# Kernel tuning notes

Hardware: AMD Instinct MI355X
Metric: run time of the kernel (lower is better)

Reference implementation:

```python
import jax, jax.numpy as jnp
import numpy as np
from jax import lax

EPS = 1e-5
TAU = 2.0
THR = 1.0

@jax.custom_vjp
def spike_fn(x):
    # torch.heaviside(x, 1.0): 1 where x >= 0, else 0
    return (x >= 0).astype(x.dtype)

def _spike_fwd(x):
    return spike_fn(x), x

def _spike_bwd(x, g):
    alpha = 4.0
    s = jax.nn.sigmoid(alpha * x)
    return (g * (1.0 - s) * s * alpha,)

spike_fn.defvjp(_spike_fwd, _spike_bwd)

def lif(x):
    # sequential membrane recurrence over dim 0 (time)
    def step(v, xt):
        v = v + (xt - v) / TAU
        s = spike_fn(v - THR)
        v = (1.0 - lax.stop_gradient(s)) * v
        return v, s
    _, spikes = lax.scan(step, jnp.zeros_like(x[0]), x)
    return spikes

def bn(x, p):
    # eval-mode BatchNorm2d; p = [weight, bias, mean, var], each [C]
    w, b, m, v = p
    inv = w / jnp.sqrt(v + EPS)
    return (x - m[None, :, None, None]) * inv[None, :, None, None] + b[None, :, None, None]

def bn_and_pad(x, p):
    # BN then pad 1 pixel on all sides with the BN-of-zero value
    w, b, m, v = p
    y = bn(x, p)
    pad_val = b - m * w / jnp.sqrt(v + EPS)  # [C]
    y = jnp.pad(y, ((0, 0), (0, 0), (1, 1), (1, 1)))
    pv = pad_val[None, :, None]  # broadcasts over batch and spatial
    y = y.at[:, :, 0, :].set(pv)
    y = y.at[:, :, -1, :].set(pv)
    y = y.at[:, :, :, 0].set(pv)
    y = y.at[:, :, :, -1].set(pv)
    return y

def branch(x, w1, dw, pw, bn3):
    # RepConv: 1x1 -> BNAndPad(1) -> depthwise3x3(valid) -> 1x1 -> BN, then outer BN
    C = x.shape[1]
    y = jnp.einsum('oc,bchw->bohw', w1, x)
    y = bn_and_pad(y, bn3[0])
    y = lax.conv_general_dilated(y, dw[:, None, :, :], (1, 1), 'VALID',
                                 dimension_numbers=('NCHW', 'OIHW', 'NCHW'),
                                 feature_group_count=C)
    y = jnp.einsum('oc,bchw->bohw', pw, y)
    y = bn(y, bn3[1])
    y = bn(y, bn3[2])
    return y

def _to_heads(t, B, N, h, d):
    # [B,C,H,W] -> [B,h,N,d]
    return t.reshape(B, h * d, N).transpose(0, 2, 1).reshape(B, N, h, d).transpose(0, 2, 1, 3)

def forward(x, q_w1, q_dw, q_pw, q_bn, k_w1, k_dw, k_pw, k_bn,
            v_w1, v_dw, v_pw, v_bn, p_w1, p_dw, p_pw, p_bn,
            num_heads=8):
    B, C, H, W = x.shape
    N = H * W
    h = num_heads
    d = C // h
    scale = float(d) ** -0.5

    xs = lif(x)
    q = lif(branch(xs, q_w1, q_dw, q_pw, q_bn))
    k = lif(branch(xs, k_w1, k_dw, k_pw, k_bn))
    v = lif(branch(xs, v_w1, v_dw, v_pw, v_bn))

    q = _to_heads(q, B, N, h, d)
    k = _to_heads(k, B, N, h, d)
    v = _to_heads(v, B, N, h, d)

    kv = jnp.einsum('bhnd,bhne->bhde', k, v)          # [B,h,d,d]
    o = jnp.einsum('bhnd,bhde->bhne', q, kv) * scale  # [B,h,N,d]
    o = o.transpose(0, 1, 3, 2).reshape(B, C, N)       # [B,C,N]
    o = lif(o)
    o = o.reshape(B, C, H, W)
    o = branch(o, p_w1, p_dw, p_pw, p_bn)
    return o.reshape(B, C, H, W)

def setup_inputs() -> dict:
    key = jax.random.key(0)
    ks = jax.random.split(key, 20)
    B, C, H, W = 8, 256, 64, 64
    s1 = 1.0 / np.sqrt(C)

    def make_bn(k):
        k1, k2, k3, k4 = jax.random.split(k, 4)
        w = 1.0 + 0.1 * jax.random.normal(k1, (3, C), jnp.float32)
        b = 0.1 * jax.random.normal(k2, (3, C), jnp.float32)
        m = 0.1 * jax.random.normal(k3, (3, C), jnp.float32)
        var = jax.random.uniform(k4, (3, C), jnp.float32, 0.5, 1.5)
        return jnp.stack([w, b, m, var], axis=1)  # [3,4,C]

    inp = {'x': jax.random.normal(ks[0], (B, C, H, W), jnp.float32)}
    for i, p in enumerate(['q', 'k', 'v', 'p']):
        kk = jax.random.split(ks[1 + i], 4)
        inp[p + '_w1'] = jax.random.normal(kk[0], (C, C), jnp.float32) * s1
        inp[p + '_dw'] = jax.random.normal(kk[1], (C, 3, 3), jnp.float32) * 0.3
        inp[p + '_pw'] = jax.random.normal(kk[2], (C, C), jnp.float32) * s1
        inp[p + '_bn'] = make_bn(kk[3])
    return inp

def reference(x, q_w1, q_dw, q_pw, q_bn, k_w1, k_dw, k_pw, k_bn,
              v_w1, v_dw, v_pw, v_bn, p_w1, p_dw, p_pw, p_bn):
    return forward(x, q_w1, q_dw, q_pw, q_bn, k_w1, k_dw, k_pw, k_bn,
                   v_w1, v_dw, v_pw, v_bn, p_w1, p_dw, p_pw, p_bn)
```

## Files before the change

### kernel.cpp

```cpp
#include <hip/hip_runtime.h>
#include <hip/hip_bf16.h>
#include <math.h>

#define T_ 8
#define C_ 256
#define N_ 4096
#define CN_ (C_ * N_)
#define EPSB 1e-5f

typedef unsigned long long u64;
typedef unsigned int u32;
typedef short bf16x8 __attribute__((ext_vector_type(8)));
typedef float f32x4 __attribute__((ext_vector_type(4)));

static __device__ __forceinline__ unsigned short f2bf(float f) {
    __hip_bfloat16 h = __float2bfloat16(f);
    return *(unsigned short*)&h;
}
static __device__ __forceinline__ float bf2f(unsigned short u) {
    u32 x = (u32)u << 16;
    return *(float*)&x;
}


__global__ __launch_bounds__(256) void lif_x_frag(const float* __restrict__ X,
                                                  unsigned short* __restrict__ ST) {
    int nb = blockIdx.x * 32;
    int c0 = blockIdx.y * 8;
    int tid = threadIdx.x;
    int nj = tid & 31, ci = tid >> 5;
    size_t base = (size_t)(c0 + ci) * N_ + nb + nj;
    __shared__ unsigned short Ls[8][34];
    int k32 = c0 >> 5, quad = (c0 >> 3) & 3;
    float v = 0.f;
#pragma unroll
    for (int t = 0; t < T_; t++) {
        float xt = X[(size_t)t * CN_ + base];
        v = v + (xt - v) / 2.0f;
        int s = (v - 1.0f >= 0.f) ? 1 : 0;
        Ls[ci][nj] = s ? (unsigned short)0x3F80 : (unsigned short)0;
        if (s) v = 0.f;
        __syncthreads();
        if (tid < 32) {
            int np = nb + tid;
            bf16x8 bs;
#pragma unroll
            for (int j = 0; j < 8; j++) bs[j] = (short)Ls[j][tid];
            *(bf16x8*)&ST[(size_t)t * CN_ +
                ((size_t)((np >> 4) * 8 + k32)) * 512 + (quad * 16 + (np & 15)) * 8] = bs;
        }
        __syncthreads();
    }
}

struct LArgs {
    const float* F[3];
    unsigned char* sq;
    u64* kbp;
    u64* vbp;
};
__global__ __launch_bounds__(256) void lif3(LArgs a) {
    int br = blockIdx.y;
    int idx = blockIdx.x * 256 + threadIdx.x;
    const float* X = a.F[br];
    int lane = threadIdx.x & 63;
    u64* BP = (br == 1) ? a.kbp : a.vbp;
    float v = 0.f;
#pragma unroll
    for (int t = 0; t < T_; t++) {
        float xt = X[(size_t)t * CN_ + idx];
        v = v + (xt - v) / 2.0f;
        int s = (v - 1.0f >= 0.f) ? 1 : 0;
        if (br == 0) {
            a.sq[(size_t)t * CN_ + idx] = (unsigned char)s;
        } else {
            u64 mask = __ballot(s);
            if (lane == 0) BP[((size_t)t * CN_ + idx) >> 6] = mask;
        }
        if (s) v = 0.f;
    }
}

struct WPtrs { const float* w[8]; };
__global__ __launch_bounds__(256) void split_w(WPtrs p, unsigned short* __restrict__ out) {
    int mat = blockIdx.y;
    int idx = blockIdx.x * 256 + threadIdx.x;
    int m = idx >> 8, k = idx & 255;
    float w = p.w[mat][idx];
    unsigned short h1 = f2bf(w);
    float f1 = bf2f(h1);
    unsigned short h2 = f2bf(w - f1);
    unsigned short h3 = f2bf(w - f1 - bf2f(h2));
    int lane = ((k >> 3) & 3) * 16 + (m & 15);
    size_t pos = ((size_t)(((m >> 4) * 8 + (k >> 5)) * 64 + lane)) * 8 + (k & 7);
    size_t base = (size_t)mat * 3 * 65536;
    out[base + pos] = h1;
    out[base + 65536 + pos] = h2;
    out[base + 2 * 65536 + pos] = h3;
}

static __device__ __forceinline__ void dw_body(const float* __restrict__ Yt,
                                               const float* __restrict__ dw,
                                               const float* __restrict__ bnp,
                                               unsigned short* __restrict__ Bh,
                                               unsigned short* __restrict__ Bl,
                                               int y0, int cg, int tid) {
    int c0 = cg * 8;
    __shared__ float L[8][6][68];
    __shared__ float invs[8], bs_[8], ms_[8], pads_[8];

    if (tid < 8) {
        int c = c0 + tid;
        float w = bnp[c], b = bnp[256 + c], m = bnp[512 + c], var = bnp[768 + c];
        float sq = sqrtf(var + EPSB);
        invs[tid] = w / sq;
        bs_[tid] = b;
        ms_[tid] = m;
        pads_[tid] = b - (m * w) / sq;
    }
    __syncthreads();

    for (int i = tid; i < 8 * 6 * 66; i += 256) {
        int c = i / 396;
        int rem = i - c * 396;
        int row = rem / 66, col = rem - row * 66;
        int gy = y0 - 1 + row, gx = col - 1;
        float val;
        if (gy < 0 || gy > 63 || gx < 0 || gx > 63) val = pads_[c];
        else val = (Yt[(size_t)(c0 + c) * N_ + gy * 64 + gx] - ms_[c]) * invs[c] + bs_[c];
        L[c][row][col] = val;
    }
    __syncthreads();

    int x = tid & 63, ry = tid >> 6;
    int n = (y0 + ry) * 64 + x;

    bf16x8 hi, lo;
#pragma unroll
    for (int j = 0; j < 8; j++) {
        const float* dwc = dw + (c0 + j) * 9;
        float a = 0.f;
#pragma unroll
        for (int dy = 0; dy < 3; dy++)
#pragma unroll
            for (int dx = 0; dx < 3; dx++)
                a += dwc[dy * 3 + dx] * L[j][ry + dy][x + dx];
        unsigned short h = f2bf(a);
        hi[j] = (short)h;
        lo[j] = (short)f2bf(a - bf2f(h));
    }
    size_t pos = ((size_t)((n >> 4) * 8 + (cg >> 2))) * 512 +
                 (size_t)(((cg & 3) * 16 + (n & 15)) * 8);
    *(bf16x8*)&Bh[pos] = hi;
    *(bf16x8*)&Bl[pos] = lo;
}

__global__ __launch_bounds__(256) void dw_bn_split(const float* __restrict__ Yin,
                                                   const float* __restrict__ dw,
                                                   const float* __restrict__ bnp,
                                                   unsigned short* __restrict__ BhT,
                                                   unsigned short* __restrict__ BlT) {
    int t = blockIdx.z;
    dw_body(Yin + (size_t)t * CN_, dw, bnp,
            BhT + (size_t)t * CN_, BlT + (size_t)t * CN_,
            blockIdx.x * 4, blockIdx.y, threadIdx.x);
}

struct DArgs {
    const float* F[3];
    const float* dw[3];
    const float* bn[3];
    unsigned short* Ph[3];
    unsigned short* Pl[3];
};
__global__ __launch_bounds__(256) void dw3(DArgs a) {
    int br = blockIdx.z >> 3, t = blockIdx.z & 7;
    dw_body(a.F[br] + (size_t)t * CN_, a.dw[br], a.bn[br],
            a.Ph[br] + (size_t)t * CN_, a.Pl[br] + (size_t)t * CN_,
            blockIdx.x * 4, blockIdx.y, threadIdx.x);
}

static __device__ __forceinline__ void gemm_s_core(const unsigned short* __restrict__ Wsp,
                                                   const unsigned short* __restrict__ Bt,
                                                   float* __restrict__ Yt,
                                                   int bx, int by, int tid) {
    int l = tid & 63, wave = tid >> 6;
    int wm = wave >> 1, wn = wave & 1;
    int lcol = l & 15, quad = l >> 4;

    f32x4 acc[4][4];
#pragma unroll
    for (int i = 0; i < 4; i++)
#pragma unroll
        for (int j = 0; j < 4; j++) acc[i][j] = (f32x4){0.f, 0.f, 0.f, 0.f};

#pragma unroll 4
    for (int k32 = 0; k32 < 8; k32++) {
        bf16x8 bfr[4];
#pragma unroll
        for (int nt = 0; nt < 4; nt++)
            bfr[nt] = *(const bf16x8*)&Bt[((size_t)((bx * 8 + wn * 4 + nt) * 8 + k32)) * 512 + l * 8];
#pragma unroll
        for (int s = 0; s < 3; s++) {
            const unsigned short* Ws = Wsp + (size_t)s * 65536;
#pragma unroll
            for (int mt = 0; mt < 4; mt++) {
                bf16x8 afr = *(const bf16x8*)&Ws[((size_t)((by * 8 + wm * 4 + mt) * 8 + k32)) * 512 + l * 8];
#pragma unroll
                for (int nt = 0; nt < 4; nt++)
                    acc[mt][nt] = __builtin_amdgcn_mfma_f32_16x16x32_bf16(
                        afr, bfr[nt], acc[mt][nt], 0, 0, 0);
            }
        }
    }

    int m0 = by * 128, n0 = bx * 128;
#pragma unroll
    for (int mt = 0; mt < 4; mt++)
#pragma unroll
        for (int i = 0; i < 4; i++) {
            int row = m0 + wm * 64 + mt * 16 + quad * 4 + i;
            float* yr = &Yt[(size_t)row * N_ + n0 + wn * 64 + lcol];
#pragma unroll
            for (int nt = 0; nt < 4; nt++) yr[nt * 16] = acc[mt][nt][i];
        }
}

static __device__ __forceinline__ void gemm_f_core(const unsigned short* __restrict__ Wsp,
                                                   const unsigned short* __restrict__ Bht,
                                                   const unsigned short* __restrict__ Blt,
                                                   float* __restrict__ Yt,
                                                   const float* __restrict__ bnp,
                                                   int bx, int by, int tid) {
    int l = tid & 63, wave = tid >> 6;
    int wm = wave >> 1, wn = wave & 1;
    int lcol = l & 15, quad = l >> 4;

    f32x4 acc[4][4];
#pragma unroll
    for (int i = 0; i < 4; i++)
#pragma unroll
        for (int j = 0; j < 4; j++) acc[i][j] = (f32x4){0.f, 0.f, 0.f, 0.f};

#pragma unroll 4
    for (int k32 = 0; k32 < 8; k32++) {
        bf16x8 bh[4], bl[4];
#pragma unroll
        for (int nt = 0; nt < 4; nt++) {
            size_t bpos = ((size_t)((bx * 8 + wn * 4 + nt) * 8 + k32)) * 512 + l * 8;
            bh[nt] = *(const bf16x8*)&Bht[bpos];
            bl[nt] = *(const bf16x8*)&Blt[bpos];
        }
#pragma unroll
        for (int s = 0; s < 3; s++) {
            const unsigned short* Ws = Wsp + (size_t)s * 65536;
#pragma unroll
            for (int mt = 0; mt < 4; mt++) {
                bf16x8 afr = *(const bf16x8*)&Ws[((size_t)((by * 8 + wm * 4 + mt) * 8 + k32)) * 512 + l * 8];
#pragma unroll
                for (int nt = 0; nt < 4; nt++)
                    acc[mt][nt] = __builtin_amdgcn_mfma_f32_16x16x32_bf16(
                        afr, bh[nt], acc[mt][nt], 0, 0, 0);
                if (s < 2) {
#pragma unroll
                    for (int nt = 0; nt < 4; nt++)
                        acc[mt][nt] = __builtin_amdgcn_mfma_f32_16x16x32_bf16(
                            afr, bl[nt], acc[mt][nt], 0, 0, 0);
                }
            }
        }
    }

    int m0 = by * 128, n0 = bx * 128;
#pragma unroll
    for (int mt = 0; mt < 4; mt++)
#pragma unroll
        for (int i = 0; i < 4; i++) {
            int row = m0 + wm * 64 + mt * 16 + quad * 4 + i;
            float i1 = bnp[1024 + row] / sqrtf(bnp[1024 + 768 + row] + EPSB);
            float b1 = bnp[1024 + 256 + row], m1 = bnp[1024 + 512 + row];
            float i2 = bnp[2048 + row] / sqrtf(bnp[2048 + 768 + row] + EPSB);
            float b2 = bnp[2048 + 256 + row], m2 = bnp[2048 + 512 + row];
            float* yr = &Yt[(size_t)row * N_ + n0 + wn * 64 + lcol];
#pragma unroll
            for (int nt = 0; nt < 4; nt++)
                yr[nt * 16] = ((acc[mt][nt][i] - m1) * i1 + b1 - m2) * i2 + b2;
        }
}

__global__ __launch_bounds__(256) void gemm_s2(const unsigned short* __restrict__ Wsp,
                                               const unsigned short* __restrict__ ST,
                                               float* __restrict__ Y) {
    int t = blockIdx.z;
    gemm_s_core(Wsp, ST + (size_t)t * CN_, Y + (size_t)t * CN_,
                blockIdx.x, blockIdx.y, threadIdx.x);
}
__global__ __launch_bounds__(256) void gemm_f2(const unsigned short* __restrict__ Wsp,
                                               const unsigned short* __restrict__ BhT,
                                               const unsigned short* __restrict__ BlT,
                                               float* __restrict__ Y,
                                               const float* __restrict__ bnp) {
    int t = blockIdx.z;
    gemm_f_core(Wsp, BhT + (size_t)t * CN_, BlT + (size_t)t * CN_,
                Y + (size_t)t * CN_, bnp, blockIdx.x, blockIdx.y, threadIdx.x);
}

struct GSArgs { const unsigned short* W[3]; const unsigned short* ST; float* F[3]; };
__global__ __launch_bounds__(256) void gemm_s3(GSArgs a) {
    int t = blockIdx.z;
    int br = blockIdx.y >> 1, byl = blockIdx.y & 1;
    gemm_s_core(a.W[br], a.ST + (size_t)t * CN_, a.F[br] + (size_t)t * CN_,
                blockIdx.x, byl, threadIdx.x);
}
struct GFArgs {
    const unsigned short* W[3];
    const unsigned short* Ph[3];
    const unsigned short* Pl[3];
    float* F[3];
    const float* bn[3];
};
__global__ __launch_bounds__(256) void gemm_f3(GFArgs a) {
    int t = blockIdx.z;
    int br = blockIdx.y >> 1, byl = blockIdx.y & 1;
    gemm_f_core(a.W[br], a.Ph[br] + (size_t)t * CN_, a.Pl[br] + (size_t)t * CN_,
                a.F[br] + (size_t)t * CN_, a.bn[br], blockIdx.x, byl, threadIdx.x);
}

__global__ __launch_bounds__(1024) void attn_kv_bp(const u64* __restrict__ Kbp,
                                                   const u64* __restrict__ Vbp,
                                                   float* __restrict__ kvbuf) {
    int th = blockIdx.x;
    int t = th >> 3, h = th & 7;
    const u64* kb = Kbp + ((size_t)t * C_ + h * 32) * 64;
    const u64* vb = Vbp + ((size_t)t * C_ + h * 32) * 64;
    __shared__ u64 ks[32][65];
    __shared__ u64 vs[32][65];
    int tid = threadIdx.x;
    {
        int r = tid >> 5, w2 = (tid & 31) * 2;
        ks[r][w2] = kb[r * 64 + w2];     ks[r][w2 + 1] = kb[r * 64 + w2 + 1];
        vs[r][w2] = vb[r * 64 + w2];     vs[r][w2 + 1] = vb[r * 64 + w2 + 1];
    }
    __syncthreads();
    int d = tid >> 5, e = tid & 31;
    int cnt = 0;
#pragma unroll
    for (int w = 0; w < 64; w++)
        cnt += __popcll(ks[d][w] & vs[e][w]);
    kvbuf[(size_t)th * 1024 + d * 32 + e] = (float)cnt;
}

__global__ __launch_bounds__(256) void attn_olif(const unsigned char* __restrict__ q,
                                                 const float* __restrict__ kvbuf,
                                                 unsigned short* __restrict__ ST) {
    int h = blockIdx.y;
    int nb = blockIdx.x * 128;
    int tid = threadIdx.x;
    int nj = tid & 127, eh = tid >> 7;
    int n = nb + nj;
    __shared__ float kvs[1024];
    const float scale = 0.17677669529663687f;
    float v[16];
#pragma unroll
    for (int e = 0; e < 16; e++) v[e] = 0.f;
    size_t posbase = ((size_t)((n >> 4) * 8 + h)) * 512 + (size_t)(n & 15) * 8;
    int quad0 = 2 * eh;
#pragma unroll
    for (int t = 0; t < T_; t++) {
        for (int i = tid; i < 1024; i += 256)
            kvs[i] = kvbuf[(size_t)(t * 8 + h) * 1024 + i];
        __syncthreads();
        float acc[16];
#pragma unroll
        for (int e = 0; e < 16; e++) acc[e] = 0.f;
        const unsigned char* qb = q + (size_t)t * CN_ + (size_t)(h * 32) * N_ + n;
#pragma unroll 4
        for (int d = 0; d < 32; d++) {
            float qd = (float)qb[(size_t)d * N_];
#pragma unroll
            for (int e = 0; e < 16; e++)
                acc[e] += qd * kvs[d * 32 + eh * 16 + e];
        }
        bf16x8 w0, w1;
#pragma unroll
        for (int e = 0; e < 16; e++) {
            float o = acc[e] * scale;
            v[e] = v[e] + (o - v[e]) / 2.0f;
            int s = (v[e] - 1.0f >= 0.f) ? 1 : 0;
            short bits = s ? (short)0x3F80 : (short)0;
            if (e < 8) w0[e] = bits; else w1[e - 8] = bits;
            if (s) v[e] = 0.f;
        }
        unsigned short* Stt = ST + (size_t)t * CN_;
        *(bf16x8*)&Stt[posbase + (size_t)(quad0 * 16) * 8] = w0;
        *(bf16x8*)&Stt[posbase + (size_t)((quad0 + 1) * 16) * 8] = w1;
        __syncthreads();
    }
}

extern "C" void kernel_launch(void* const* d_in, const int* in_sizes, int n_in,
                              void* d_out, int out_size, void* d_ws, size_t ws_size,
                              hipStream_t stream) {
    const float* x = (const float*)d_in[0];
    const float* q_w1 = (const float*)d_in[1];
    const float* q_dw = (const float*)d_in[2];
    const float* q_pw = (const float*)d_in[3];
    const float* q_bn = (const float*)d_in[4];
    const float* k_w1 = (const float*)d_in[5];
    const float* k_dw = (const float*)d_in[6];
    const float* k_pw = (const float*)d_in[7];
    const float* k_bn = (const float*)d_in[8];
    const float* v_w1 = (const float*)d_in[9];
    const float* v_dw = (const float*)d_in[10];
    const float* v_pw = (const float*)d_in[11];
    const float* v_bn = (const float*)d_in[12];
    const float* p_w1 = (const float*)d_in[13];
    const float* p_dw = (const float*)d_in[14];
    const float* p_pw = (const float*)d_in[15];
    const float* p_bn = (const float*)d_in[16];

    const size_t SZ = (size_t)T_ * CN_;
    float* out = (float*)d_out;
    float* F0 = (float*)d_ws;
    float* F1 = F0 + SZ;
    float* F2 = F1 + SZ;
    float* P0 = F2 + SZ;
    float* P1 = P0 + SZ;
    float* P2 = P1 + SZ;
    float* bufKV = P2 + SZ;
    unsigned char* xs = (unsigned char*)(bufKV + 65536);
    unsigned char* sq = xs + SZ;
    u64* kbp = (u64*)(sq + SZ);
    u64* vbp = kbp + (SZ >> 6);
    unsigned short* wspA = (unsigned short*)(vbp + (SZ >> 6));
    unsigned short* ST = wspA + 8 * 3 * 65536;

    unsigned short* P0h = (unsigned short*)P0; unsigned short* P0l = P0h + SZ;
    unsigned short* P1h = (unsigned short*)P1; unsigned short* P1l = P1h + SZ;
    unsigned short* P2h = (unsigned short*)P2; unsigned short* P2l = P2h + SZ;

    WPtrs wp;
    wp.w[0] = q_w1; wp.w[1] = q_pw; wp.w[2] = k_w1; wp.w[3] = k_pw;
    wp.w[4] = v_w1; wp.w[5] = v_pw; wp.w[6] = p_w1; wp.w[7] = p_pw;
    split_w<<<dim3(256, 8), dim3(256), 0, stream>>>(wp, wspA);
    const size_t WS3 = 3 * 65536;

    lif_x_frag<<<dim3(N_ / 32, C_ / 8), dim3(256), 0, stream>>>(x, ST);

    GSArgs gs;
    gs.W[0] = wspA + 0 * WS3; gs.W[1] = wspA + 2 * WS3; gs.W[2] = wspA + 4 * WS3;
    gs.ST = ST; gs.F[0] = F0; gs.F[1] = F1; gs.F[2] = F2;
    gemm_s3<<<dim3(N_ / 128, 6, T_), dim3(256), 0, stream>>>(gs);

    DArgs da;
    da.F[0] = F0; da.F[1] = F1; da.F[2] = F2;
    da.dw[0] = q_dw; da.dw[1] = k_dw; da.dw[2] = v_dw;
    da.bn[0] = q_bn; da.bn[1] = k_bn; da.bn[2] = v_bn;
    da.Ph[0] = P0h; da.Ph[1] = P1h; da.Ph[2] = P2h;
    da.Pl[0] = P0l; da.Pl[1] = P1l; da.Pl[2] = P2l;
    dw3<<<dim3(16, 32, 3 * T_), dim3(256), 0, stream>>>(da);

    GFArgs gf;
    gf.W[0] = wspA + 1 * WS3; gf.W[1] = wspA + 3 * WS3; gf.W[2] = wspA + 5 * WS3;
    gf.Ph[0] = P0h; gf.Ph[1] = P1h; gf.Ph[2] = P2h;
    gf.Pl[0] = P0l; gf.Pl[1] = P1l; gf.Pl[2] = P2l;
    gf.F[0] = F0; gf.F[1] = F1; gf.F[2] = F2;
    gf.bn[0] = q_bn; gf.bn[1] = k_bn; gf.bn[2] = v_bn;
    gemm_f3<<<dim3(N_ / 128, 6, T_), dim3(256), 0, stream>>>(gf);

    LArgs la;
    la.F[0] = F0; la.F[1] = F1; la.F[2] = F2;
    la.sq = sq; la.kbp = kbp; la.vbp = vbp;
    lif3<<<dim3(CN_ / 256, 3), dim3(256), 0, stream>>>(la);

    attn_kv_bp<<<dim3(64), dim3(1024), 0, stream>>>(kbp, vbp, bufKV);
    attn_olif<<<dim3(N_ / 128, 8), dim3(256), 0, stream>>>(sq, bufKV, ST);

    gemm_s2<<<dim3(N_ / 128, C_ / 128, T_), dim3(256), 0, stream>>>(wspA + 6 * WS3, ST, out);
    dw_bn_split<<<dim3(16, 32, T_), dim3(256), 0, stream>>>(out, p_dw, p_bn, P0h, P0l);
    gemm_f2<<<dim3(N_ / 128, C_ / 128, T_), dim3(256), 0, stream>>>(wspA + 7 * WS3, P0h, P0l, out, p_bn);
}
```

Baseline: 442.9 us.

## Stage GEMM A/B fragments in LDS via global_load_lds in both GEMM cores

Both the spike GEMM and the float-split GEMM now stage each k-step's weight and activation fragments in shared memory. The four waves share the copy work through direct global-to-LDS loads, then read their fragments from LDS. Before, each wave fetched its fragments straight from global memory, so fragments used by two waves in a block were loaded twice; staging is meant to remove that redundant traffic. In exchange it adds two block barriers per k-step, there is no double-buffering so load latency is no longer overlapped with MFMA, and the unroll pragma is removed.

```diff
diff --git a/kernel.cpp b/kernel.cpp
--- a/kernel.cpp
+++ b/kernel.cpp
@@ -20,6 +20,13 @@
 static __device__ __forceinline__ float bf2f(unsigned short u) {
     u32 x = (u32)u << 16;
     return *(float*)&x;
+}
+
+typedef const __attribute__((address_space(1))) unsigned int ga_u32;
+typedef __attribute__((address_space(3))) unsigned int la_u32;
+static __device__ __forceinline__ void gl_lds16(const unsigned short* g,
+                                                unsigned short* l_) {
+    __builtin_amdgcn_global_load_lds((ga_u32*)g, (la_u32*)l_, 16, 0, 0);
 }
 
 
@@ -188,30 +195,48 @@
     int wm = wave >> 1, wn = wave & 1;
     int lcol = l & 15, quad = l >> 4;
 
+    __shared__ unsigned short As[24][512];
+    __shared__ unsigned short Bs[8][512];
+
     f32x4 acc[4][4];
 #pragma unroll
     for (int i = 0; i < 4; i++)
 #pragma unroll
         for (int j = 0; j < 4; j++) acc[i][j] = (f32x4){0.f, 0.f, 0.f, 0.f};
 
-#pragma unroll 4
     for (int k32 = 0; k32 < 8; k32++) {
+#pragma unroll
+        for (int i = 0; i < 8; i++) {
+            int tau = wave * 8 + i;
+            if (tau < 24) {
+                int s = tau >> 3, mtg = tau & 7;
+                gl_lds16(&Wsp[(size_t)s * 65536 +
+                              ((size_t)((by * 8 + mtg) * 8 + k32)) * 512 + l * 8],
+                         &As[tau][0]);
+            } else {
+                int nt = tau - 24;
+                gl_lds16(&Bt[((size_t)((bx * 8 + nt) * 8 + k32)) * 512 + l * 8],
+                         &Bs[nt][0]);
+            }
+        }
+        __syncthreads();
+
         bf16x8 bfr[4];
 #pragma unroll
         for (int nt = 0; nt < 4; nt++)
-            bfr[nt] = *(const bf16x8*)&Bt[((size_t)((bx * 8 + wn * 4 + nt) * 8 + k32)) * 512 + l * 8];
+            bfr[nt] = *(const bf16x8*)&Bs[wn * 4 + nt][l * 8];
 #pragma unroll
         for (int s = 0; s < 3; s++) {
-            const unsigned short* Ws = Wsp + (size_t)s * 65536;
 #pragma unroll
             for (int mt = 0; mt < 4; mt++) {
-                bf16x8 afr = *(const bf16x8*)&Ws[((size_t)((by * 8 + wm * 4 + mt) * 8 + k32)) * 512 + l * 8];
+                bf16x8 afr = *(const bf16x8*)&As[s * 8 + wm * 4 + mt][l * 8];
 #pragma unroll
                 for (int nt = 0; nt < 4; nt++)
                     acc[mt][nt] = __builtin_amdgcn_mfma_f32_16x16x32_bf16(
                         afr, bfr[nt], acc[mt][nt], 0, 0, 0);
             }
         }
+        __syncthreads();
     }
 
     int m0 = by * 128, n0 = bx * 128;
@@ -236,27 +261,48 @@
     int wm = wave >> 1, wn = wave & 1;
     int lcol = l & 15, quad = l >> 4;
 
+    __shared__ unsigned short As[24][512];
+    __shared__ unsigned short Bhs[8][512];
+    __shared__ unsigned short Bls[8][512];
+
     f32x4 acc[4][4];
 #pragma unroll
     for (int i = 0; i < 4; i++)
 #pragma unroll
         for (int j = 0; j < 4; j++) acc[i][j] = (f32x4){0.f, 0.f, 0.f, 0.f};
 
-#pragma unroll 4
     for (int k32 = 0; k32 < 8; k32++) {
+#pragma unroll
+        for (int i = 0; i < 10; i++) {
+            int tau = wave * 10 + i;
+            if (tau < 24) {
+                int s = tau >> 3, mtg = tau & 7;
+                gl_lds16(&Wsp[(size_t)s * 65536 +
+                              ((size_t)((by * 8 + mtg) * 8 + k32)) * 512 + l * 8],
+                         &As[tau][0]);
+            } else if (tau < 32) {
+                int nt = tau - 24;
+                gl_lds16(&Bht[((size_t)((bx * 8 + nt) * 8 + k32)) * 512 + l * 8],
+                         &Bhs[nt][0]);
+            } else {
+                int nt = tau - 32;
+                gl_lds16(&Blt[((size_t)((bx * 8 + nt) * 8 + k32)) * 512 + l * 8],
+                         &Bls[nt][0]);
+            }
+        }
+        __syncthreads();
+
         bf16x8 bh[4], bl[4];
 #pragma unroll
         for (int nt = 0; nt < 4; nt++) {
-            size_t bpos = ((size_t)((bx * 8 + wn * 4 + nt) * 8 + k32)) * 512 + l * 8;
-            bh[nt] = *(const bf16x8*)&Bht[bpos];
-            bl[nt] = *(const bf16x8*)&Blt[bpos];
+            bh[nt] = *(const bf16x8*)&Bhs[wn * 4 + nt][l * 8];
+            bl[nt] = *(const bf16x8*)&Bls[wn * 4 + nt][l * 8];
         }
 #pragma unroll
         for (int s = 0; s < 3; s++) {
-            const unsigned short* Ws = Wsp + (size_t)s * 65536;
 #pragma unroll
             for (int mt = 0; mt < 4; mt++) {
-                bf16x8 afr = *(const bf16x8*)&Ws[((size_t)((by * 8 + wm * 4 + mt) * 8 + k32)) * 512 + l * 8];
+                bf16x8 afr = *(const bf16x8*)&As[s * 8 + wm * 4 + mt][l * 8];
 #pragma unroll
                 for (int nt = 0; nt < 4; nt++)
                     acc[mt][nt] = __builtin_amdgcn_mfma_f32_16x16x32_bf16(
@@ -269,6 +315,7 @@
                 }
             }
         }
+        __syncthreads();
     }
 
     int m0 = by * 128, n0 = bx * 128;
```

Result: faster. 413.4 us (-6.7%).
